# Kernel optimization log

Hardware: AMD Instinct MI355X
Metric: run time of the kernel (lower is better)

The kernel has to match this reference:

```python
import jax, jax.numpy as jnp
import numpy as np

B, T, D = 4, 2048, 1024
DK, DV = 1024, 1024
BETA1, BETA2 = 1.0, 1.0
EPS = 1e-12  # torch F.normalize eps


def setup_inputs() -> dict:
    key = jax.random.key(0)
    kx, kq, kk, kv, ko = jax.random.split(key, 5)
    def w(k, shape):
        return jax.random.normal(k, shape, dtype=jnp.float32) * (shape[0] ** -0.5)
    return {
        "x": jax.random.normal(kx, (B, T, D), dtype=jnp.float32),
        # Weights stored [in, out]; torch Linear is x @ W.T with W [out, in] -- equivalent math.
        "Wq": w(kq, (D, DK)),
        "Wk": w(kk, (D, DK)),
        "Wv": w(kv, (D, DV)),
        "Wo": w(ko, (DV, D)),
    }


def reference(x, Wq, Wk, Wv, Wo):
    scale = DK ** -0.5
    q = (x @ Wq) * scale                      # [B,T,DK]
    k = x @ Wk
    k = k / jnp.maximum(jnp.linalg.norm(k, axis=-1, keepdims=True), EPS)
    v = x @ Wv                                # [B,T,DV]
    # time-major for scan
    qT = jnp.swapaxes(q, 0, 1)
    kT = jnp.swapaxes(k, 0, 1)
    vT = jnp.swapaxes(v, 0, 1)
    S0 = jnp.zeros((B, DV, DK), dtype=x.dtype)

    def step(S, qkv_t):
        q_t, k_t, v_t = qkv_t                 # each [B, d]
        # S @ (I - b1 k k^T) = S - b1 (S k) k^T   (same math, rank-1 form)
        Sk = jnp.einsum('bvk,bk->bv', S, k_t)
        S = S - BETA1 * Sk[:, :, None] * k_t[:, None, :] \
              + BETA2 * v_t[:, :, None] * k_t[:, None, :]
        o_t = jnp.einsum('bvk,bk->bv', S, q_t)
        return S, o_t

    _, oT = jax.lax.scan(step, S0, (qT, kT, vT))  # oT: [T,B,DV]
    out = jnp.swapaxes(oT, 0, 1) @ Wo             # [B,T,D]
    return out
```

## Files before the change

kernel.cpp:

```cpp
#include <hip/hip_runtime.h>

typedef unsigned short u16;
typedef __attribute__((ext_vector_type(8))) short short8;
typedef __attribute__((ext_vector_type(4))) float floatx4;

#define B_ 4
#define T_ 2048
#define CH 64

__device__ __forceinline__ u16 f2bf(float f) {
  unsigned int x = __float_as_uint(f);
  return (u16)((x + 0x7FFFu + ((x >> 16) & 1u)) >> 16);
}
__device__ __forceinline__ float bf2f(u16 u) {
  union { unsigned int i; float f; } v; v.i = ((unsigned int)u) << 16; return v.f;
}

__device__ __forceinline__ void barrier_lgkm() {
  asm volatile("s_waitcnt lgkmcnt(0)\n\ts_barrier" ::: "memory");
}

__global__ __launch_bounds__(256) void xconv_kernel(const float* __restrict__ x,
                                                    u16* __restrict__ Xbf) {
  size_t idx = ((size_t)blockIdx.x * 256 + threadIdx.x) * 4;
  float4 v = *reinterpret_cast<const float4*>(&x[idx]);
  ushort4 o;
  o.x = f2bf(v.x); o.y = f2bf(v.y); o.z = f2bf(v.z); o.w = f2bf(v.w);
  *reinterpret_cast<ushort4*>(&Xbf[idx]) = o;
}

__global__ __launch_bounds__(256) void wtrans_kernel(
    const float* __restrict__ W0, const float* __restrict__ W1,
    const float* __restrict__ W2, const float* __restrict__ W3,
    u16* __restrict__ T0, u16* __restrict__ T1,
    u16* __restrict__ T2, u16* __restrict__ T3)
{
  const int z = blockIdx.z;
  const float* W = (z == 0) ? W0 : (z == 1) ? W1 : (z == 2) ? W2 : W3;
  u16* T = (z == 0) ? T0 : (z == 1) ? T1 : (z == 2) ? T2 : T3;
  const int k0 = blockIdx.x * 64, n0 = blockIdx.y * 64;
  const int tid = threadIdx.x;
  __shared__ float Tile[64][65];
#pragma unroll
  for (int i = 0; i < 4; ++i) {
    int lin = tid + i * 256;
    int r = lin >> 4, c4 = (lin & 15) * 4;
    *reinterpret_cast<float4*>(&Tile[r][c4]) =
        *reinterpret_cast<const float4*>(&W[(size_t)(k0 + r) * 1024 + n0 + c4]);
  }
  __syncthreads();
#pragma unroll
  for (int i = 0; i < 4; ++i) {
    int lin = tid + i * 256;
    int r = lin >> 4, c4 = (lin & 15) * 4;
    ushort4 o;
    o.x = f2bf(Tile[c4 + 0][r]); o.y = f2bf(Tile[c4 + 1][r]);
    o.z = f2bf(Tile[c4 + 2][r]); o.w = f2bf(Tile[c4 + 3][r]);
    *reinterpret_cast<ushort4*>(&T[(size_t)(n0 + r) * 1024 + k0 + c4]) = o;
  }
}

__global__ __launch_bounds__(256) void mgemm_qkv(
    const u16* __restrict__ Xbf,
    const u16* __restrict__ WqT, const u16* __restrict__ WkT, const u16* __restrict__ WvT,
    u16* __restrict__ Qbf, u16* __restrict__ Kbf, u16* __restrict__ Vbf,
    int tg, int lsh)
{
  const int z = blockIdx.z;
  const u16* BT = (z == 0) ? WqT : ((z == 1) ? WkT : WvT);
  u16* O = (z == 0) ? Qbf : ((z == 1) ? Kbf : Vbf);
  const float scale = (z == 0) ? 0.03125f : 1.0f;
  const int r0 = blockIdx.x * 128, c0 = blockIdx.y * 128;
  const int tid = threadIdx.x;
  const int lane = tid & 63, wave = tid >> 6;
  const int quad = lane >> 4, l16 = lane & 15;
  const int wr = (wave >> 1) * 64, wc = (wave & 1) * 64;

  __shared__ u16 As[128][40];
  __shared__ u16 Bs[128][40];

  const int ar = tid >> 1, ac = (tid & 1) * 16;
  const int lr = r0 + ar;
  const int agrow = ((lr >> lsh) << 11) + tg + (lr & ((1 << lsh) - 1));
  const u16* aptr = &Xbf[(size_t)agrow * 1024 + ac];
  const u16* bptr = &BT[(size_t)(c0 + ar) * 1024 + ac];

  floatx4 acc[4][4] = {};
  for (int k0 = 0; k0 < 1024; k0 += 32) {
    float4 av0 = *reinterpret_cast<const float4*>(aptr + k0);
    float4 av1 = *reinterpret_cast<const float4*>(aptr + k0 + 8);
    float4 bv0 = *reinterpret_cast<const float4*>(bptr + k0);
    float4 bv1 = *reinterpret_cast<const float4*>(bptr + k0 + 8);
    __syncthreads();
    *reinterpret_cast<float4*>(&As[ar][ac]) = av0;
    *reinterpret_cast<float4*>(&As[ar][ac + 8]) = av1;
    *reinterpret_cast<float4*>(&Bs[ar][ac]) = bv0;
    *reinterpret_cast<float4*>(&Bs[ar][ac + 8]) = bv1;
    __syncthreads();
    short8 afr[4], bfr[4];
#pragma unroll
    for (int i = 0; i < 4; ++i) {
      afr[i] = *reinterpret_cast<const short8*>(&As[wr + i * 16 + l16][quad * 8]);
      bfr[i] = *reinterpret_cast<const short8*>(&Bs[wc + i * 16 + l16][quad * 8]);
    }
#pragma unroll
    for (int mi = 0; mi < 4; ++mi)
#pragma unroll
      for (int ni = 0; ni < 4; ++ni)
        acc[mi][ni] = __builtin_amdgcn_mfma_f32_16x16x32_bf16(afr[mi], bfr[ni], acc[mi][ni], 0, 0, 0);
  }
#pragma unroll
  for (int mi = 0; mi < 4; ++mi)
#pragma unroll
    for (int reg = 0; reg < 4; ++reg) {
      int row = r0 + wr + mi * 16 + quad * 4 + reg;
#pragma unroll
      for (int ni = 0; ni < 4; ++ni) {
        int col = c0 + wc + ni * 16 + l16;
        O[(size_t)row * 1024 + col] = f2bf(acc[mi][ni][reg] * scale);
      }
    }
}

__global__ __launch_bounds__(256) void mgemm_out(
    const u16* __restrict__ Obf, const u16* __restrict__ WoT,
    float* __restrict__ out, int tg, int lsh)
{
  const int r0 = blockIdx.x * 128, c0 = blockIdx.y * 128;
  const int tid = threadIdx.x;
  const int lane = tid & 63, wave = tid >> 6;
  const int quad = lane >> 4, l16 = lane & 15;
  const int wr = (wave >> 1) * 64, wc = (wave & 1) * 64;

  __shared__ u16 As[128][40];
  __shared__ u16 Bs[128][40];

  const int ar = tid >> 1, ac = (tid & 1) * 16;
  const u16* aptr = &Obf[(size_t)(r0 + ar) * 1024 + ac];
  const u16* bptr = &WoT[(size_t)(c0 + ar) * 1024 + ac];

  floatx4 acc[4][4] = {};
  for (int k0 = 0; k0 < 1024; k0 += 32) {
    float4 av0 = *reinterpret_cast<const float4*>(aptr + k0);
    float4 av1 = *reinterpret_cast<const float4*>(aptr + k0 + 8);
    float4 bv0 = *reinterpret_cast<const float4*>(bptr + k0);
    float4 bv1 = *reinterpret_cast<const float4*>(bptr + k0 + 8);
    __syncthreads();
    *reinterpret_cast<float4*>(&As[ar][ac]) = av0;
    *reinterpret_cast<float4*>(&As[ar][ac + 8]) = av1;
    *reinterpret_cast<float4*>(&Bs[ar][ac]) = bv0;
    *reinterpret_cast<float4*>(&Bs[ar][ac + 8]) = bv1;
    __syncthreads();
    short8 afr[4], bfr[4];
#pragma unroll
    for (int i = 0; i < 4; ++i) {
      afr[i] = *reinterpret_cast<const short8*>(&As[wr + i * 16 + l16][quad * 8]);
      bfr[i] = *reinterpret_cast<const short8*>(&Bs[wc + i * 16 + l16][quad * 8]);
    }
#pragma unroll
    for (int mi = 0; mi < 4; ++mi)
#pragma unroll
      for (int ni = 0; ni < 4; ++ni)
        acc[mi][ni] = __builtin_amdgcn_mfma_f32_16x16x32_bf16(afr[mi], bfr[ni], acc[mi][ni], 0, 0, 0);
  }
#pragma unroll
  for (int mi = 0; mi < 4; ++mi)
#pragma unroll
    for (int reg = 0; reg < 4; ++reg) {
      int lr = r0 + wr + mi * 16 + quad * 4 + reg;
      int grow = ((lr >> lsh) << 11) + tg + (lr & ((1 << lsh) - 1));
#pragma unroll
      for (int ni = 0; ni < 4; ++ni) {
        int col = c0 + wc + ni * 16 + l16;
        out[(size_t)grow * 1024 + col] = acc[mi][ni][reg];
      }
    }
}

__global__ __launch_bounds__(256) void knorm_kernel(u16* __restrict__ Kbf) {
  const int row = blockIdx.x;
  const int tid = threadIdx.x;
  ushort4 v4 = *reinterpret_cast<const ushort4*>(&Kbf[(size_t)row * 1024 + tid * 4]);
  float a = bf2f(v4.x), b = bf2f(v4.y), c = bf2f(v4.z), d = bf2f(v4.w);
  float ss = a * a + b * b + c * c + d * d;
#pragma unroll
  for (int off = 32; off > 0; off >>= 1) ss += __shfl_down(ss, off);
  __shared__ float wsum[4];
  if ((tid & 63) == 0) wsum[tid >> 6] = ss;
  __syncthreads();
  float tot = wsum[0] + wsum[1] + wsum[2] + wsum[3];
  float inv = 1.0f / fmaxf(sqrtf(tot), 1e-12f);
  ushort4 o;
  o.x = f2bf(a * inv); o.y = f2bf(b * inv); o.z = f2bf(c * inv); o.w = f2bf(d * inv);
  *reinterpret_cast<ushort4*>(&Kbf[(size_t)row * 1024 + tid * 4]) = o;
}

__global__ __launch_bounds__(256) void ktrans_kernel(const u16* __restrict__ Kbf,
                                                     u16* __restrict__ KT,
                                                     int tgs) {
  const int t0 = blockIdx.x * 64;
  const int d0 = blockIdx.y * 64;
  const int b = blockIdx.z;
  const int tid = threadIdx.x;
  __shared__ u16 Tile[64][68];
#pragma unroll
  for (int i = 0; i < 4; ++i) {
    int lin = tid + i * 256;
    int r = lin >> 4, c4 = (lin & 15) * 4;
    *reinterpret_cast<ushort4*>(&Tile[r][c4]) =
        *reinterpret_cast<const ushort4*>(&Kbf[(size_t)(b * tgs + t0 + r) * 1024 + d0 + c4]);
  }
  __syncthreads();
#pragma unroll
  for (int i = 0; i < 4; ++i) {
    int lin = tid + i * 256;
    int r = lin >> 4, c4 = (lin & 15) * 4;
    ushort4 o;
    o.x = Tile[c4 + 0][r]; o.y = Tile[c4 + 1][r];
    o.z = Tile[c4 + 2][r]; o.w = Tile[c4 + 3][r];
    *reinterpret_cast<ushort4*>(&KT[((size_t)b * 1024 + d0 + r) * tgs + t0 + c4]) = o;
  }
}

__global__ __launch_bounds__(256) void attn_winv_kernel(
    const u16* __restrict__ Qbf, const u16* __restrict__ Kbf,
    u16* __restrict__ Pb, u16* __restrict__ Wb, int tgs)
{
  const int cc = blockIdx.x;
  const int b = blockIdx.y;
  const int base = b * tgs + cc * CH;
  const int tid = threadIdx.x;
  const int lane = tid & 63;
  const int wave = tid >> 6;
  const int quad = lane >> 4, l16 = lane & 15;
  const int m0 = wave * 16;

  __shared__ float Asm[64][64];
  __shared__ float Wsm[64][65];

  floatx4 accA[4] = {};
  floatx4 accP[4] = {};
  const u16* arowK = &Kbf[(size_t)(base + m0 + l16) * 1024];
  const u16* arowQ = &Qbf[(size_t)(base + m0 + l16) * 1024];
#pragma unroll 4
  for (int kk = 0; kk < 32; ++kk) {
    short8 aK = *reinterpret_cast<const short8*>(&arowK[kk * 32 + quad * 8]);
    short8 aQ = *reinterpret_cast<const short8*>(&arowQ[kk * 32 + quad * 8]);
#pragma unroll
    for (int nt = 0; nt < 4; ++nt) {
      short8 bK = *reinterpret_cast<const short8*>(
          &Kbf[(size_t)(base + nt * 16 + l16) * 1024 + kk * 32 + quad * 8]);
      accA[nt] = __builtin_amdgcn_mfma_f32_16x16x32_bf16(aK, bK, accA[nt], 0, 0, 0);
      accP[nt] = __builtin_amdgcn_mfma_f32_16x16x32_bf16(aQ, bK, accP[nt], 0, 0, 0);
    }
  }
  const size_t pw0 = ((size_t)(cc * B_ + b) * CH) * 64;
#pragma unroll
  for (int nt = 0; nt < 4; ++nt) {
#pragma unroll
    for (int reg = 0; reg < 4; ++reg) {
      int t = m0 + quad * 4 + reg;
      int i = nt * 16 + l16;
      Asm[t][i] = (i < t) ? accA[nt][reg] : 0.0f;
      Pb[pw0 + (size_t)t * 64 + i] = f2bf((i <= t) ? accP[nt][reg] : 0.0f);
    }
  }
  __syncthreads();

  if (tid < 64) {
    const int j = tid;
    for (int t = 0; t < 64; ++t) {
      float s = (t == j) ? 1.0f : 0.0f;
      for (int i = 0; i < t; ++i) s -= Asm[t][i] * Wsm[i][j];
      Wsm[t][j] = s;
    }
    for (int t = 0; t < 64; ++t)
      Wb[pw0 + (size_t)t * 64 + j] = f2bf(Wsm[t][j]);
  }
}

__global__ __launch_bounds__(512, 2) void chain_kernel(
    const u16* __restrict__ Qbf, const u16* __restrict__ Kbf,
    const u16* __restrict__ KT, const u16* __restrict__ Vbf,
    u16* __restrict__ Obf, const u16* __restrict__ Wb, const u16* __restrict__ Pb,
    float* __restrict__ Sglob, int lsh, int cpg, int g, int ngrp)
{
  const int wg = blockIdx.x;
  const int t8 = wg & 7;
  const int b = t8 >> 1;
  const int sl = ((wg >> 3) << 1) | (t8 & 1);
  const int c0 = sl * 16;
  const int tgs = 1 << lsh;
  const int tid = threadIdx.x;
  const int lane = tid & 63;
  const int wave = tid >> 6;
  const int quad = lane >> 4, l16 = lane & 15;
  const int d0w = wave * 128;
  const bool isK = (wave < 4);
  const int m0 = (isK ? wave : (wave - 4)) * 16;

  __shared__ u16 Sb[16][1048];
  __shared__ u16 rhsT[16][88];
  __shared__ u16 uT[16][88];

  floatx4 Sreg[8];
  if (g == 0) {
#pragma unroll
    for (int nt = 0; nt < 8; ++nt) Sreg[nt] = (floatx4){0.f, 0.f, 0.f, 0.f};
    for (int idx = tid; idx < 16 * 256; idx += 512) {
      int r = idx >> 8, d4 = (idx & 255) * 4;
      ushort4 z4 = {0, 0, 0, 0};
      *reinterpret_cast<ushort4*>(&Sb[r][d4]) = z4;
    }
  } else {
#pragma unroll
    for (int nt = 0; nt < 8; ++nt)
#pragma unroll
      for (int reg = 0; reg < 4; ++reg)
        Sreg[nt][reg] = Sglob[((size_t)b * 1024 + c0 + quad * 4 + reg) * 1024 +
                              d0w + nt * 16 + l16];
    for (int idx = tid; idx < 16 * 1024; idx += 512) {
      int r = idx >> 10, d = idx & 1023;
      Sb[r][d] = f2bf(Sglob[((size_t)b * 1024 + c0 + r) * 1024 + d]);
    }
  }
  __syncthreads();

  const u16* const Abase = isK ? Kbf : Qbf;
  const u16* arow = Abase + (size_t)(b * tgs + m0 + l16) * 1024;
  short8 pa0 = *reinterpret_cast<const short8*>(arow + 0 * 32 + quad * 8);
  short8 pa1 = *reinterpret_cast<const short8*>(arow + 1 * 32 + quad * 8);
  short8 pa2 = *reinterpret_cast<const short8*>(arow + 2 * 32 + quad * 8);
  short8 pa3 = *reinterpret_cast<const short8*>(arow + 3 * 32 + quad * 8);

  for (int cc = 0; cc < cpg; ++cc) {
    const int base = b * tgs + cc * CH;
    const size_t pw0 = ((size_t)(cc * B_ + b) * CH) * 64;

    float vv[4];
    if (isK) {
#pragma unroll
      for (int reg = 0; reg < 4; ++reg)
        vv[reg] = bf2f(Vbf[(size_t)(base + m0 + quad * 4 + reg) * 1024 + c0 + l16]);
    }
    short8 wpf0, wpf1;
    {
      const u16* row = (isK ? Wb : Pb) + pw0 + (size_t)(m0 + l16) * 64;
      wpf0 = *reinterpret_cast<const short8*>(row + quad * 8);
      wpf1 = *reinterpret_cast<const short8*>(row + 32 + quad * 8);
    }

    short8 ktf[8][2];
    floatx4 ac0 = {}, ac1 = {}, ac2 = {}, ac3 = {};
#pragma unroll
    for (int kk8 = 0; kk8 < 8; ++kk8) {
      const int kb = kk8 * 4;
      {
        const u16* ktrow = &KT[((size_t)b * 1024 + d0w + kk8 * 16 + l16) * tgs + cc * CH];
        ktf[kk8][0] = *reinterpret_cast<const short8*>(ktrow + quad * 8);
        ktf[kk8][1] = *reinterpret_cast<const short8*>(ktrow + 32 + quad * 8);
      }
      const u16* nap = (kk8 < 7) ? (arow + (kb + 4) * 32)
                                 : (arow + (cc + 1 < cpg ? CH * 1024 : 0));
      short8 na0 = *reinterpret_cast<const short8*>(nap + 0 * 32 + quad * 8);
      short8 na1 = *reinterpret_cast<const short8*>(nap + 1 * 32 + quad * 8);
      short8 na2 = *reinterpret_cast<const short8*>(nap + 2 * 32 + quad * 8);
      short8 na3 = *reinterpret_cast<const short8*>(nap + 3 * 32 + quad * 8);
      short8 b0 = *reinterpret_cast<const short8*>(&Sb[l16][(kb + 0) * 32 + quad * 8]);
      short8 b1 = *reinterpret_cast<const short8*>(&Sb[l16][(kb + 1) * 32 + quad * 8]);
      short8 b2 = *reinterpret_cast<const short8*>(&Sb[l16][(kb + 2) * 32 + quad * 8]);
      short8 b3 = *reinterpret_cast<const short8*>(&Sb[l16][(kb + 3) * 32 + quad * 8]);
      ac0 = __builtin_amdgcn_mfma_f32_16x16x32_bf16(pa0, b0, ac0, 0, 0, 0);
      ac1 = __builtin_amdgcn_mfma_f32_16x16x32_bf16(pa1, b1, ac1, 0, 0, 0);
      ac2 = __builtin_amdgcn_mfma_f32_16x16x32_bf16(pa2, b2, ac2, 0, 0, 0);
      ac3 = __builtin_amdgcn_mfma_f32_16x16x32_bf16(pa3, b3, ac3, 0, 0, 0);
      pa0 = na0; pa1 = na1; pa2 = na2; pa3 = na3;
    }
    floatx4 accS = (ac0 + ac1) + (ac2 + ac3);

    asm volatile("" ::
      "v"(ktf[0][0]), "v"(ktf[0][1]), "v"(ktf[1][0]), "v"(ktf[1][1]),
      "v"(ktf[2][0]), "v"(ktf[2][1]), "v"(ktf[3][0]), "v"(ktf[3][1]),
      "v"(ktf[4][0]), "v"(ktf[4][1]), "v"(ktf[5][0]), "v"(ktf[5][1]),
      "v"(ktf[6][0]), "v"(ktf[6][1]), "v"(ktf[7][0]), "v"(ktf[7][1]));

    if (isK) {
#pragma unroll
      for (int reg = 0; reg < 4; ++reg)
        rhsT[l16][m0 + quad * 4 + reg] = f2bf(vv[reg] - accS[reg]);
    }
    barrier_lgkm();

    if (isK) {
      floatx4 uacc = {};
      short8 br0 = *reinterpret_cast<const short8*>(&rhsT[l16][quad * 8]);
      short8 br1 = *reinterpret_cast<const short8*>(&rhsT[l16][32 + quad * 8]);
      uacc = __builtin_amdgcn_mfma_f32_16x16x32_bf16(wpf0, br0, uacc, 0, 0, 0);
      uacc = __builtin_amdgcn_mfma_f32_16x16x32_bf16(wpf1, br1, uacc, 0, 0, 0);
#pragma unroll
      for (int reg = 0; reg < 4; ++reg)
        uT[l16][m0 + quad * 4 + reg] = f2bf(uacc[reg]);
    }
    barrier_lgkm();

    if (!isK) {
      floatx4 oacc = accS;
      short8 bu0 = *reinterpret_cast<const short8*>(&uT[l16][quad * 8]);
      short8 bu1 = *reinterpret_cast<const short8*>(&uT[l16][32 + quad * 8]);
      oacc = __builtin_amdgcn_mfma_f32_16x16x32_bf16(wpf0, bu0, oacc, 0, 0, 0);
      oacc = __builtin_amdgcn_mfma_f32_16x16x32_bf16(wpf1, bu1, oacc, 0, 0, 0);
#pragma unroll
      for (int reg = 0; reg < 4; ++reg) {
        int t = m0 + quad * 4 + reg;
        Obf[(size_t)(base + t) * 1024 + c0 + l16] = f2bf(oacc[reg]);
      }
    }

    {
      short8 ua0 = *reinterpret_cast<const short8*>(&uT[l16][quad * 8]);
      short8 ua1 = *reinterpret_cast<const short8*>(&uT[l16][32 + quad * 8]);
#pragma unroll
      for (int nt = 0; nt < 8; ++nt) {
        floatx4 cf = Sreg[nt];
        cf = __builtin_amdgcn_mfma_f32_16x16x32_bf16(ua0, ktf[nt][0], cf, 0, 0, 0);
        cf = __builtin_amdgcn_mfma_f32_16x16x32_bf16(ua1, ktf[nt][1], cf, 0, 0, 0);
        Sreg[nt] = cf;
        const int dn = d0w + nt * 16;
#pragma unroll
        for (int reg = 0; reg < 4; ++reg)
          Sb[quad * 4 + reg][dn + l16] = f2bf(cf[reg]);
      }
    }
    barrier_lgkm();
    arow += CH * 1024;
  }

  if (g < ngrp - 1) {
#pragma unroll
    for (int nt = 0; nt < 8; ++nt)
#pragma unroll
      for (int reg = 0; reg < 4; ++reg)
        Sglob[((size_t)b * 1024 + c0 + quad * 4 + reg) * 1024 + d0w + nt * 16 + l16] =
            Sreg[nt][reg];
  }
}

extern "C" void kernel_launch(void* const* d_in, const int* in_sizes, int n_in,
                              void* d_out, int out_size, void* d_ws, size_t ws_size,
                              hipStream_t stream) {
  const float* x  = (const float*)d_in[0];
  const float* Wq = (const float*)d_in[1];
  const float* Wk = (const float*)d_in[2];
  const float* Wv = (const float*)d_in[3];
  const float* Wo = (const float*)d_in[4];
  float* out = (float*)d_out;

  int lsh = 8;
  {
    const int cand[4] = {11, 10, 9, 8};
    for (int i = 0; i < 4; ++i) {
      size_t tgs = (size_t)1 << cand[i];
      size_t C = (size_t)B_ * tgs * 1024;
      size_t cpg = tgs / CH;
      size_t need = (size_t)B_ * T_ * 1024 * 2
                  + 4 * ((size_t)1024 * 1024 * 2)
                  + 5 * (C * 2)
                  + 2 * (cpg * B_ * CH * 64 * 2)
                  + (size_t)B_ * 1024 * 1024 * 4
                  + 32768;
      if (need <= ws_size) { lsh = cand[i]; break; }
    }
  }
  const int tgs = 1 << lsh;
  const int cpg = tgs / CH;
  const int ngrp = T_ / tgs;
  const int rows = B_ * tgs;

  char* ws = (char*)d_ws;
  size_t off = 0;
  auto alloc = [&](size_t bytes) -> void* {
    void* p = ws + off;
    off += (bytes + 255) & ~(size_t)255;
    return p;
  };
  u16* Xbf = (u16*)alloc((size_t)B_ * T_ * 1024 * 2);
  u16* WqT = (u16*)alloc((size_t)1024 * 1024 * 2);
  u16* WkT = (u16*)alloc((size_t)1024 * 1024 * 2);
  u16* WvT = (u16*)alloc((size_t)1024 * 1024 * 2);
  u16* WoT = (u16*)alloc((size_t)1024 * 1024 * 2);
  u16* Qbf = (u16*)alloc((size_t)rows * 1024 * 2);
  u16* Kbf = (u16*)alloc((size_t)rows * 1024 * 2);
  u16* Vbf = (u16*)alloc((size_t)rows * 1024 * 2);
  u16* KT  = (u16*)alloc((size_t)rows * 1024 * 2);
  u16* Obf = (u16*)alloc((size_t)rows * 1024 * 2);
  u16* Pb  = (u16*)alloc((size_t)cpg * B_ * CH * 64 * 2);
  u16* Wb  = (u16*)alloc((size_t)cpg * B_ * CH * 64 * 2);
  float* Sglob = (float*)alloc((size_t)B_ * 1024 * 1024 * 4);

  xconv_kernel<<<B_ * T_, 256, 0, stream>>>(x, Xbf);
  wtrans_kernel<<<dim3(16, 16, 4), 256, 0, stream>>>(Wq, Wk, Wv, Wo, WqT, WkT, WvT, WoT);

  for (int g = 0; g < ngrp; ++g) {
    int tg = g * tgs;
    mgemm_qkv<<<dim3(rows / 128, 8, 3), 256, 0, stream>>>(Xbf, WqT, WkT, WvT,
                                                          Qbf, Kbf, Vbf, tg, lsh);
    knorm_kernel<<<rows, 256, 0, stream>>>(Kbf);
    ktrans_kernel<<<dim3(tgs / 64, 16, B_), 256, 0, stream>>>(Kbf, KT, tgs);
    attn_winv_kernel<<<dim3(cpg, B_), 256, 0, stream>>>(Qbf, Kbf, Pb, Wb, tgs);
    chain_kernel<<<256, 512, 0, stream>>>(Qbf, Kbf, KT, Vbf, Obf, Wb, Pb, Sglob,
                                          lsh, cpg, g, ngrp);
    mgemm_out<<<dim3(rows / 128, 8), 256, 0, stream>>>(Obf, WoT, out, tg, lsh);
  }
}
```

Before: 642.6 us.

## Hand-schedule global loads with inline asm and explicit vmcnt waits in the chunk scan

Replaces compiler-generated loads in the recurrent chunk loop with inline-asm global_load instructions that use immediate offsets, manual s_waitcnt vmcnt counts and sched_barrier fences. The Q/K row fragments are prefetched two k-steps ahead through an 8-slot register ring, and KT, W/P and V loads are interleaved across the first iterations. Output stores also become inline asm. The aim is to hide global load latency on the serial per-chunk critical path. In exchange, the hard-coded vmcnt values must exactly match the issue order, so any mismatch risks reading registers before their loads complete, and the larger ring adds register pressure.

```diff
diff --git a/kernel.cpp b/kernel.cpp
--- a/kernel.cpp
+++ b/kernel.cpp
@@ -19,6 +19,45 @@
 __device__ __forceinline__ void barrier_lgkm() {
   asm volatile("s_waitcnt lgkmcnt(0)\n\ts_barrier" ::: "memory");
 }
+
+#define GL(dst, addr, IMM) \
+  asm volatile("global_load_dwordx4 %0, %1, off offset:" #IMM : "=v"(dst) : "v"(addr))
+#define GLU(dst, addr, IMM) \
+  asm volatile("global_load_ushort %0, %1, off offset:" #IMM : "=v"(dst) : "v"(addr))
+#define GS(addr, val, IMM) \
+  asm volatile("global_store_short %0, %1, off offset:" #IMM :: "v"(addr), "v"(val))
+
+#define GLA(slot, base, I0, I1, I2, I3) do { \
+  GL(af[slot][0], base, I0); GL(af[slot][1], base, I1); \
+  GL(af[slot][2], base, I2); GL(af[slot][3], base, I3); } while (0)
+
+#define GLKT(nt0) do { \
+  const u16* kp0_ = ktb + (size_t)(nt0) * ktstep; \
+  GL(ktf[nt0][0], kp0_, 0); GL(ktf[nt0][1], kp0_, 64); \
+  const u16* kp1_ = ktb + (size_t)(nt0 + 1) * ktstep; \
+  GL(ktf[nt0 + 1][0], kp1_, 0); GL(ktf[nt0 + 1][1], kp1_, 64); } while (0)
+
+#define GLX4 do { \
+  GL(wpf0, wrow, 0); GL(wpf1, wrow, 64); \
+  GLU(vv0, vvb, 0); GLU(vv1, vvb, 2048); \
+  GLU(vv2, vvb2, 0); GLU(vv3, vvb2, 2048); } while (0)
+
+#define NOOP ((void)0)
+
+#define AITER(K, NW, PREFETCH, XCODE) do { \
+  asm volatile("s_waitcnt vmcnt(" #NW ")"); \
+  __builtin_amdgcn_sched_barrier(0x387); \
+  PREFETCH; \
+  XCODE; \
+  short8 b0_ = *reinterpret_cast<const short8*>(&Sb[l16][(K * 4 + 0) * 32 + quad * 8]); \
+  short8 b1_ = *reinterpret_cast<const short8*>(&Sb[l16][(K * 4 + 1) * 32 + quad * 8]); \
+  short8 b2_ = *reinterpret_cast<const short8*>(&Sb[l16][(K * 4 + 2) * 32 + quad * 8]); \
+  short8 b3_ = *reinterpret_cast<const short8*>(&Sb[l16][(K * 4 + 3) * 32 + quad * 8]); \
+  ac0 = __builtin_amdgcn_mfma_f32_16x16x32_bf16(af[K][0], b0_, ac0, 0, 0, 0); \
+  ac1 = __builtin_amdgcn_mfma_f32_16x16x32_bf16(af[K][1], b1_, ac1, 0, 0, 0); \
+  ac2 = __builtin_amdgcn_mfma_f32_16x16x32_bf16(af[K][2], b2_, ac2, 0, 0, 0); \
+  ac3 = __builtin_amdgcn_mfma_f32_16x16x32_bf16(af[K][3], b3_, ac3, 0, 0, 0); \
+} while (0)
 
 __global__ __launch_bounds__(256) void xconv_kernel(const float* __restrict__ x,
                                                     u16* __restrict__ Xbf) {
@@ -298,6 +337,7 @@
   const int d0w = wave * 128;
   const bool isK = (wave < 4);
   const int m0 = (isK ? wave : (wave - 4)) * 16;
+  const size_t ktstep = (size_t)16 * tgs;
 
   __shared__ u16 Sb[16][1048];
   __shared__ u16 rhsT[16][88];
@@ -328,66 +368,50 @@
 
   const u16* const Abase = isK ? Kbf : Qbf;
   const u16* arow = Abase + (size_t)(b * tgs + m0 + l16) * 1024;
-  short8 pa0 = *reinterpret_cast<const short8*>(arow + 0 * 32 + quad * 8);
-  short8 pa1 = *reinterpret_cast<const short8*>(arow + 1 * 32 + quad * 8);
-  short8 pa2 = *reinterpret_cast<const short8*>(arow + 2 * 32 + quad * 8);
-  short8 pa3 = *reinterpret_cast<const short8*>(arow + 3 * 32 + quad * 8);
+
+  short8 af[8][4];
+  short8 ktf[8][2];
+  short8 wpf0, wpf1;
+  unsigned int vv0, vv1, vv2, vv3;
+
+  {
+    const u16* aq0 = arow + quad * 8;
+    GLA(0, aq0, 0, 64, 128, 192);
+    GLA(1, aq0, 256, 320, 384, 448);
+  }
 
   for (int cc = 0; cc < cpg; ++cc) {
     const int base = b * tgs + cc * CH;
     const size_t pw0 = ((size_t)(cc * B_ + b) * CH) * 64;
 
-    float vv[4];
+    const u16* aq   = arow + quad * 8;
+    const u16* aqn  = arow + (size_t)(cc + 1 < cpg ? CH * 1024 : 0) + quad * 8;
+    const u16* ktb  = KT + ((size_t)b * 1024 + d0w + l16) * tgs + (size_t)cc * CH + quad * 8;
+    const u16* wrow = (isK ? Wb : Pb) + pw0 + (size_t)(m0 + l16) * 64 + quad * 8;
+    const u16* vvb  = Vbf + (size_t)(base + m0 + quad * 4) * 1024 + c0 + l16;
+    const u16* vvb2 = vvb + 2048;
+
+    floatx4 ac0 = {}, ac1 = {}, ac2 = {}, ac3 = {};
+
+    AITER(0, 4,  GLA(2, aq, 512, 576, 640, 704),     GLKT(0));
+    AITER(1, 8,  GLA(3, aq, 768, 832, 896, 960),     GLKT(2));
+    AITER(2, 12, GLA(4, aq, 1024, 1088, 1152, 1216), GLKT(4));
+    AITER(3, 12, GLA(5, aq, 1280, 1344, 1408, 1472), GLKT(6));
+    AITER(4, 12, GLA(6, aq, 1536, 1600, 1664, 1728), GLX4);
+    AITER(5, 14, GLA(7, aq, 1792, 1856, 1920, 1984), NOOP);
+    AITER(6, 10, GLA(0, aqn, 0, 64, 128, 192),       NOOP);
+    AITER(7, 4,  GLA(1, aqn, 256, 320, 384, 448),    NOOP);
+
+    asm volatile("s_waitcnt vmcnt(12)");
+    __builtin_amdgcn_sched_barrier(0);
+
+    floatx4 accS = (ac0 + ac1) + (ac2 + ac3);
+
     if (isK) {
-#pragma unroll
-      for (int reg = 0; reg < 4; ++reg)
-        vv[reg] = bf2f(Vbf[(size_t)(base + m0 + quad * 4 + reg) * 1024 + c0 + l16]);
-    }
-    short8 wpf0, wpf1;
-    {
-      const u16* row = (isK ? Wb : Pb) + pw0 + (size_t)(m0 + l16) * 64;
-      wpf0 = *reinterpret_cast<const short8*>(row + quad * 8);
-      wpf1 = *reinterpret_cast<const short8*>(row + 32 + quad * 8);
-    }
-
-    short8 ktf[8][2];
-    floatx4 ac0 = {}, ac1 = {}, ac2 = {}, ac3 = {};
-#pragma unroll
-    for (int kk8 = 0; kk8 < 8; ++kk8) {
-      const int kb = kk8 * 4;
-      {
-        const u16* ktrow = &KT[((size_t)b * 1024 + d0w + kk8 * 16 + l16) * tgs + cc * CH];
-        ktf[kk8][0] = *reinterpret_cast<const short8*>(ktrow + quad * 8);
-        ktf[kk8][1] = *reinterpret_cast<const short8*>(ktrow + 32 + quad * 8);
-      }
-      const u16* nap = (kk8 < 7) ? (arow + (kb + 4) * 32)
-                                 : (arow + (cc + 1 < cpg ? CH * 1024 : 0));
-      short8 na0 = *reinterpret_cast<const short8*>(nap + 0 * 32 + quad * 8);
-      short8 na1 = *reinterpret_cast<const short8*>(nap + 1 * 32 + quad * 8);
-      short8 na2 = *reinterpret_cast<const short8*>(nap + 2 * 32 + quad * 8);
-      short8 na3 = *reinterpret_cast<const short8*>(nap + 3 * 32 + quad * 8);
-      short8 b0 = *reinterpret_cast<const short8*>(&Sb[l16][(kb + 0) * 32 + quad * 8]);
-      short8 b1 = *reinterpret_cast<const short8*>(&Sb[l16][(kb + 1) * 32 + quad * 8]);
-      short8 b2 = *reinterpret_cast<const short8*>(&Sb[l16][(kb + 2) * 32 + quad * 8]);
-      short8 b3 = *reinterpret_cast<const short8*>(&Sb[l16][(kb + 3) * 32 + quad * 8]);
-      ac0 = __builtin_amdgcn_mfma_f32_16x16x32_bf16(pa0, b0, ac0, 0, 0, 0);
-      ac1 = __builtin_amdgcn_mfma_f32_16x16x32_bf16(pa1, b1, ac1, 0, 0, 0);
-      ac2 = __builtin_amdgcn_mfma_f32_16x16x32_bf16(pa2, b2, ac2, 0, 0, 0);
-      ac3 = __builtin_amdgcn_mfma_f32_16x16x32_bf16(pa3, b3, ac3, 0, 0, 0);
-      pa0 = na0; pa1 = na1; pa2 = na2; pa3 = na3;
-    }
-    floatx4 accS = (ac0 + ac1) + (ac2 + ac3);
-
-    asm volatile("" ::
-      "v"(ktf[0][0]), "v"(ktf[0][1]), "v"(ktf[1][0]), "v"(ktf[1][1]),
-      "v"(ktf[2][0]), "v"(ktf[2][1]), "v"(ktf[3][0]), "v"(ktf[3][1]),
-      "v"(ktf[4][0]), "v"(ktf[4][1]), "v"(ktf[5][0]), "v"(ktf[5][1]),
-      "v"(ktf[6][0]), "v"(ktf[6][1]), "v"(ktf[7][0]), "v"(ktf[7][1]));
-
-    if (isK) {
-#pragma unroll
-      for (int reg = 0; reg < 4; ++reg)
-        rhsT[l16][m0 + quad * 4 + reg] = f2bf(vv[reg] - accS[reg]);
+      rhsT[l16][m0 + quad * 4 + 0] = f2bf(bf2f((u16)vv0) - accS[0]);
+      rhsT[l16][m0 + quad * 4 + 1] = f2bf(bf2f((u16)vv1) - accS[1]);
+      rhsT[l16][m0 + quad * 4 + 2] = f2bf(bf2f((u16)vv2) - accS[2]);
+      rhsT[l16][m0 + quad * 4 + 3] = f2bf(bf2f((u16)vv3) - accS[3]);
     }
     barrier_lgkm();
 
@@ -409,11 +433,12 @@
       short8 bu1 = *reinterpret_cast<const short8*>(&uT[l16][32 + quad * 8]);
       oacc = __builtin_amdgcn_mfma_f32_16x16x32_bf16(wpf0, bu0, oacc, 0, 0, 0);
       oacc = __builtin_amdgcn_mfma_f32_16x16x32_bf16(wpf1, bu1, oacc, 0, 0, 0);
-#pragma unroll
-      for (int reg = 0; reg < 4; ++reg) {
-        int t = m0 + quad * 4 + reg;
-        Obf[(size_t)(base + t) * 1024 + c0 + l16] = f2bf(oacc[reg]);
-      }
+      u16* ob  = Obf + (size_t)(base + m0 + quad * 4) * 1024 + c0 + l16;
+      u16* ob2 = ob + 2048;
+      unsigned int s0 = f2bf(oacc[0]), s1 = f2bf(oacc[1]);
+      unsigned int s2 = f2bf(oacc[2]), s3 = f2bf(oacc[3]);
+      GS(ob, s0, 0);  GS(ob, s1, 2048);
+      GS(ob2, s2, 0); GS(ob2, s3, 2048);
     }
 
     {
```

New measurement: 628.1 us. 1.02x faster.
